# Kernel tuning notes

Hardware: AMD Instinct MI355X
Metric: run time of the kernel (lower is better)

The kernel has to match this reference:

```python
import jax, jax.numpy as jnp
import numpy as np
from jax import lax

HID, STATE, K, EXPAND = 1024, 16, 4, 2
INNER = EXPAND * HID
B_SZ, L = 4, 4096


def setup_inputs() -> dict:
    key = jax.random.key(0)
    ks = jax.random.split(key, 16)
    s = 0.02
    return {
        "x": jax.random.normal(ks[0], (B_SZ, L, HID), dtype=jnp.float32),
        "in_proj_w": jax.random.normal(ks[1], (2 * INNER, HID), dtype=jnp.float32) * s,
        "in_proj_b": jnp.zeros((2 * INNER,), jnp.float32),
        "conv_w": jax.random.normal(ks[2], (INNER, 1, K), dtype=jnp.float32) * s,
        "conv_b": jnp.zeros((INNER,), jnp.float32),
        "dt_w": jax.random.normal(ks[3], (INNER, INNER), dtype=jnp.float32) * s,
        "dt_b": jnp.zeros((INNER,), jnp.float32),
        "A_log": jnp.log(jnp.abs(jax.random.normal(ks[4], (INNER, STATE), dtype=jnp.float32)) + 1e-6),
        "B_w": jax.random.normal(ks[5], (STATE, INNER), dtype=jnp.float32) * s,
        "B_b": jnp.zeros((STATE,), jnp.float32),
        "C_w": jax.random.normal(ks[6], (STATE, INNER), dtype=jnp.float32) * s,
        "C_b": jnp.zeros((STATE,), jnp.float32),
        "D": jnp.ones((INNER,), jnp.float32),
        "out_w": jax.random.normal(ks[7], (HID, INNER), dtype=jnp.float32) * s,
        "out_b": jnp.zeros((HID,), jnp.float32),
    }


def _selective_scan(x, dt, A, Bm, Cm, D):
    # x, dt: (B, L, inner); A: (inner, state); Bm, Cm: (B, L, state); D: (inner,)
    def step(h, inp):
        x_t, dt_t, B_t, C_t = inp  # (B,inner),(B,inner),(B,state),(B,state)
        dA = jnp.exp(dt_t[:, :, None] * A[None, :, :])          # (B, inner, state)
        dB = dt_t[:, :, None] * B_t[:, None, :]                  # (B, inner, state)
        h = dA * h + dB * x_t[:, :, None]
        y = jnp.einsum("bds,bs->bd", h, C_t) + D * x_t
        return h, y

    B_, _, d = x.shape
    h0 = jnp.zeros((B_, d, A.shape[1]), x.dtype)
    xs = (jnp.swapaxes(x, 0, 1), jnp.swapaxes(dt, 0, 1),
          jnp.swapaxes(Bm, 0, 1), jnp.swapaxes(Cm, 0, 1))
    _, ys = lax.scan(step, h0, xs)  # ys: (L, B, inner)
    return jnp.swapaxes(ys, 0, 1)


def reference(x, in_proj_w, in_proj_b, conv_w, conv_b, dt_w, dt_b,
              A_log, B_w, B_b, C_w, C_b, D, out_w, out_b):
    xz = x @ in_proj_w.T + in_proj_b                 # (B, L, 2*inner)
    x_part, z = jnp.split(xz, 2, axis=-1)
    # causal depthwise conv1d: torch pads both sides K-1 then truncates to L -> left pad only
    xc = lax.conv_general_dilated(
        jnp.swapaxes(x_part, 1, 2), conv_w,
        window_strides=(1,), padding=[(K - 1, 0)],
        dimension_numbers=("NCH", "OIH", "NCH"),
        feature_group_count=INNER) + conv_b[None, :, None]
    x_conv = jax.nn.silu(jnp.swapaxes(xc, 1, 2))     # (B, L, inner)
    A = -jnp.exp(A_log)
    dt = jax.nn.softplus(x_conv @ dt_w.T + dt_b)
    Bm = x_conv @ B_w.T + B_b                        # (B, L, state)
    Cm = x_conv @ C_w.T + C_b
    y = _selective_scan(x_conv, dt, A, Bm, Cm, D)
    y = y * jax.nn.silu(z)
    return y @ out_w.T + out_b
```

## Files before the change

kernel.cpp:

```cpp
#include <hip/hip_runtime.h>
#include <hip/hip_bf16.h>

#define HID   1024
#define STATE 16
#define KCONV 4
#define INNER 2048
#define BSZ   4
#define LSEQ  4096
#define BL    (BSZ * LSEQ)
#define NCAT  2176
#define NCH   64
#define TC    64

typedef unsigned short ushort_t;
typedef unsigned int   uint_t;
typedef __attribute__((ext_vector_type(8))) __bf16 bf16x8;
typedef __attribute__((ext_vector_type(4))) float  f32x4;
typedef __attribute__((ext_vector_type(8))) unsigned short u16x8;

__device__ __forceinline__ ushort_t f2bf(float f) {
    uint_t u = __float_as_uint(f);
    u += 0x7fffu + ((u >> 16) & 1u);
    return (ushort_t)(u >> 16);
}
__device__ __forceinline__ float bf2f(ushort_t h) {
    return __uint_as_float(((uint_t)h) << 16);
}

#define AS1 __attribute__((address_space(1)))
#define AS3 __attribute__((address_space(3)))
__device__ __forceinline__ void async_copy16(const ushort_t* g, ushort_t* l) {
    __builtin_amdgcn_global_load_lds((const AS1 void*)g, (AS3 void*)l, 16, 0, 0);
}

__global__ void cast_bf16_kernel(const float* __restrict__ src, ushort_t* __restrict__ dst, int n) {
    int i = blockIdx.x * 256 + threadIdx.x;
    if (i < n) dst[i] = f2bf(src[i]);
}

__global__ void build_wcat_kernel(const float* __restrict__ dtw, const float* __restrict__ Bw,
                                  const float* __restrict__ Cw, ushort_t* __restrict__ out) {
    int i = blockIdx.x * 256 + threadIdx.x;
    if (i >= NCAT * INNER) return;
    int r = i >> 11;
    int k = i & (INNER - 1);
    float v = 0.f;
    if (r < INNER)            v = dtw[i];
    else if (r < INNER + 16)  v = Bw[(r - INNER) * INNER + k];
    else if (r < INNER + 32)  v = Cw[(r - INNER - 16) * INNER + k];
    out[i] = f2bf(v);
}

__global__ void build_biascat_kernel(const float* __restrict__ dtb, const float* __restrict__ Bb,
                                     const float* __restrict__ Cb, float* __restrict__ out) {
    int i = blockIdx.x * 256 + threadIdx.x;
    if (i >= NCAT) return;
    float v = 0.f;
    if (i < INNER)            v = dtb[i];
    else if (i < INNER + 16)  v = Bb[i - INNER];
    else if (i < INNER + 32)  v = Cb[i - INNER - 16];
    out[i] = v;
}

#define mfma_bf16 __builtin_amdgcn_mfma_f32_16x16x32_bf16

template <int MODE, int KK>
__global__ __launch_bounds__(512, 2) void gemm256_kernel(
    const ushort_t* __restrict__ A, const ushort_t* __restrict__ Bw,
    const float* __restrict__ bias,
    ushort_t* __restrict__ oU0, ushort_t* __restrict__ oU1,
    float* __restrict__ oF, float* __restrict__ oB, float* __restrict__ oC,
    int N)
{
    __shared__ ushort_t smem[49152];

    const int tid  = threadIdx.x;
    const int w    = tid >> 6;
    const int lane = tid & 63;
    const int m16  = lane & 15;
    const int ko   = lane >> 4;
    const int wm   = w >> 2;
    const int wn   = w & 3;

    const int gx   = gridDim.x;
    const int lb   = blockIdx.y * gx + blockIdx.x;
    const int xcd  = lb & 7;
    const int slot = lb >> 3;
    const int tx   = slot % gx;
    const int ty   = xcd * 8 + slot / gx;
    const int row0 = ty * 256;
    const int col0 = tx * 128;

    constexpr int NKT = KK >> 6;

    const size_t Lofs = (size_t)(w * 16 + (lane >> 3)) * KK
                      + (size_t)(((lane & 7) ^ (lane >> 3)) << 3);
    const ushort_t* pA = A  + (size_t)row0 * KK + Lofs;
    const ushort_t* pB = Bw + (size_t)col0 * KK + Lofs;

    f32x4 acc[8][2] = {};

    auto stage_tile = [&](int tau) {
        const int bb = (tau & 1) * 24576;
        const int k0 = tau << 6;
#pragma unroll
        for (int j = 0; j < 3; j++) {
            const ushort_t* px = (j == 0) ? pB : pA + (size_t)((j - 1) << 7) * KK;
#pragma unroll
            for (int i = 0; i < 2; i++) {
                const ushort_t* s = px + (size_t)(i * 8) * KK + k0;
                async_copy16(s, &smem[bb + j * 8192 + w * 1024 + i * 512]);
            }
        }
    };
    auto ldA = [&](int buf, int rf, int s) -> bf16x8 {
        const int row = (rf << 4) + m16;
        const int c16 = ((s << 2) + ko) ^ (row & 7);
        return *(const bf16x8*)&smem[buf * 24576 + (1 + wm) * 8192 + (row << 6) + (c16 << 3)];
    };
    auto ldB = [&](int buf, int cf, int s) -> bf16x8 {
        const int row = (wn << 5) + (cf << 4) + m16;
        const int c16 = ((s << 2) + ko) ^ (row & 7);
        return *(const bf16x8*)&smem[buf * 24576 + (row << 6) + (c16 << 3)];
    };

    stage_tile(0);
    asm volatile("s_waitcnt vmcnt(0)" ::: "memory");
    __builtin_amdgcn_s_barrier();

#pragma unroll 1
    for (int t = 0; t < NKT; ++t) {
        const int buf = t & 1;
        if (t + 1 < NKT) stage_tile(t + 1);

#pragma unroll
        for (int s = 0; s < 2; s++) {
            const bf16x8 b0 = ldB(buf, 0, s);
            const bf16x8 b1 = ldB(buf, 1, s);
#pragma unroll
            for (int rf = 0; rf < 8; rf++) {
                const bf16x8 a = ldA(buf, rf, s);
                acc[rf][0] = mfma_bf16(a, b0, acc[rf][0], 0, 0, 0);
                acc[rf][1] = mfma_bf16(a, b1, acc[rf][1], 0, 0, 0);
            }
        }
        if (t + 1 < NKT) {
            asm volatile("s_waitcnt vmcnt(0)" ::: "memory");
            __builtin_amdgcn_s_barrier();
        }
    }

    const int rbase = (lane >> 4) * 4;
    __syncthreads();

    if (MODE == 2) {
#pragma unroll
        for (int rf = 0; rf < 8; rf++)
#pragma unroll
            for (int cf = 0; cf < 2; cf++)
#pragma unroll
                for (int r = 0; r < 4; r++) {
                    int row = row0 + wm * 128 + rf * 16 + rbase + r;
                    int col = col0 + wn * 32 + cf * 16 + m16;
                    oF[(size_t)row * N + col] = acc[rf][cf][r] + bias[col];
                }
    } else if (MODE == 1 && col0 >= INNER) {
#pragma unroll
        for (int rf = 0; rf < 8; rf++)
#pragma unroll
            for (int cf = 0; cf < 2; cf++)
#pragma unroll
                for (int r = 0; r < 4; r++) {
                    int row = row0 + wm * 128 + rf * 16 + rbase + r;
                    int col = col0 + wn * 32 + cf * 16 + m16;
                    float v = acc[rf][cf][r] + bias[col];
                    if (col < INNER + 16)      oB[(size_t)row * STATE + (col - INNER)] = v;
                    else if (col < INNER + 32) oC[(size_t)row * STATE + (col - INNER - 16)] = v;
                }
    } else {
        const bool isZ = (MODE == 0) && (col0 >= INNER);
        ushort_t* my = &smem[w * 4608];
        const int SW = 36;
#pragma unroll
        for (int rf = 0; rf < 8; rf++)
#pragma unroll
            for (int cf = 0; cf < 2; cf++)
#pragma unroll
                for (int r = 0; r < 4; r++) {
                    int lr = rf * 16 + rbase + r;
                    int lc = cf * 16 + m16;
                    float v = acc[rf][cf][r] + bias[col0 + wn * 32 + lc];
                    ushort_t o;
                    if (MODE == 0) {
                        if (isZ) { float s = v / (1.f + __expf(-v)); o = f2bf(s); }
                        else     { o = f2bf(v); }
                    } else {
                        float sp = fmaxf(v, 0.f) + log1pf(__expf(-fabsf(v)));
                        o = f2bf(sp);
                    }
                    my[lr * SW + lc] = o;
                }
        __builtin_amdgcn_sched_barrier(0);
#pragma unroll
        for (int it = 0; it < 8; it++) {
            int lr = it * 16 + (lane >> 2);
            u16x8 vv = *(const u16x8*)&my[lr * SW + (lane & 3) * 8];
            int grow = row0 + wm * 128 + lr;
            int gcol = col0 + wn * 32 + (lane & 3) * 8;
            if (MODE == 0 && isZ)
                *(u16x8*)&oU1[(size_t)grow * INNER + (gcol - INNER)] = vv;
            else
                *(u16x8*)&oU0[(size_t)grow * INNER + gcol] = vv;
        }
    }
}

__global__ void conv_silu_kernel(const ushort_t* __restrict__ xp, const float* __restrict__ cw,
                                 const float* __restrict__ cb,
                                 ushort_t* __restrict__ xcbf) {
    int i = blockIdx.x * 256 + threadIdx.x;
    int base = i * 8;
    int d0 = base & (INNER - 1);
    int bl = base >> 11;
    int l  = bl & (LSEQ - 1);

    f32x4 wv[8];
    float acc[8];
#pragma unroll
    for (int j = 0; j < 8; j++) {
        wv[j]  = *(const f32x4*)&cw[(d0 + j) * KCONV];
        acc[j] = cb[d0 + j];
    }
#pragma unroll
    for (int k = 0; k < KCONV; k++) {
        int ls = l - (KCONV - 1) + k;
        if (ls >= 0) {
            u16x8 v = *(const u16x8*)&xp[base + (ls - l) * INNER];
#pragma unroll
            for (int j = 0; j < 8; j++) acc[j] = fmaf(wv[j][k], bf2f(v[j]), acc[j]);
        }
    }
    u16x8 o;
#pragma unroll
    for (int j = 0; j < 8; j++) {
        float s = acc[j] / (1.f + __expf(-acc[j]));
        o[j] = f2bf(s);
    }
    *(u16x8*)&xcbf[base] = o;
}

__global__ __launch_bounds__(256) void scan_pass1(
    const ushort_t* __restrict__ dt, const ushort_t* __restrict__ xc,
    const float* __restrict__ Bm, const float* __restrict__ A_log,
    ushort_t* __restrict__ Pc, float* __restrict__ Sc)
{
    const int b = blockIdx.z;
    const int c = blockIdx.y;
    const int d = blockIdx.x * 256 + threadIdx.x;

    float A[STATE], h[STATE];
    {
        float al[STATE];
#pragma unroll
        for (int q = 0; q < 4; q++)
            *(f32x4*)(al + q * 4) = *(const f32x4*)(A_log + (size_t)d * STATE + q * 4);
#pragma unroll
        for (int s = 0; s < STATE; s++) { A[s] = -__expf(al[s]); h[s] = 0.f; }
    }
    float sdt = 0.f;
    const size_t base = (size_t)b * LSEQ + (size_t)c * TC;

#pragma unroll 2
    for (int t = 0; t < TC; t++) {
        const size_t r = base + t;
        const float dtv = bf2f(dt[r * INNER + d]);
        const float xv  = bf2f(xc[r * INNER + d]);
        const float dtx = dtv * xv;
        float Bv[STATE];
#pragma unroll
        for (int q = 0; q < 4; q++)
            *(f32x4*)(Bv + q * 4) = *(const f32x4*)(Bm + r * STATE + q * 4);
        sdt += dtv;
#pragma unroll
        for (int s = 0; s < STATE; s++) {
            const float dA = __expf(dtv * A[s]);
            h[s] = fmaf(dA, h[s], dtx * Bv[s]);
        }
    }

    const size_t idx = ((size_t)(b * NCH + c) * INNER + d) * STATE;
#pragma unroll
    for (int q = 0; q < 4; q++)
        *(f32x4*)(Sc + idx + q * 4) = *(const f32x4*)(h + q * 4);
    u16x8 p0, p1;
#pragma unroll
    for (int s = 0; s < 8; s++) { p0[s] = f2bf(__expf(A[s] * sdt)); }
#pragma unroll
    for (int s = 0; s < 8; s++) { p1[s] = f2bf(__expf(A[s + 8] * sdt)); }
    *(u16x8*)(Pc + idx)     = p0;
    *(u16x8*)(Pc + idx + 8) = p1;
}

__global__ __launch_bounds__(256) void scan_pass2(
    const ushort_t* __restrict__ Pc, float* Sc)
{
    const int i = blockIdx.x * 256 + threadIdx.x;
    const int b   = i >> 15;
    const int rem = i & (INNER * STATE - 1);
    float H = 0.f;
#pragma unroll 8
    for (int c = 0; c < NCH; c++) {
        const size_t idx = (size_t)(b * NCH + c) * (INNER * STATE) + rem;
        const float Pv = bf2f(Pc[idx]);
        const float Sv = Sc[idx];
        const float Hn = fmaf(Pv, H, Sv);
        Sc[idx] = H;
        H = Hn;
    }
}

__global__ __launch_bounds__(256) void scan_pass3(
    const ushort_t* __restrict__ dt, const ushort_t* __restrict__ xc,
    const float* __restrict__ Bm, const float* __restrict__ Cm,
    const float* __restrict__ A_log, const float* __restrict__ Dv,
    const float* __restrict__ Hc, ushort_t* sz_y)
{
    const int b = blockIdx.z;
    const int c = blockIdx.y;
    const int d = blockIdx.x * 256 + threadIdx.x;

    float A[STATE], h[STATE];
    {
        float al[STATE];
#pragma unroll
        for (int q = 0; q < 4; q++)
            *(f32x4*)(al + q * 4) = *(const f32x4*)(A_log + (size_t)d * STATE + q * 4);
#pragma unroll
        for (int s = 0; s < STATE; s++) A[s] = -__expf(al[s]);
    }
    const size_t hidx = ((size_t)(b * NCH + c) * INNER + d) * STATE;
#pragma unroll
    for (int q = 0; q < 4; q++)
        *(f32x4*)(h + q * 4) = *(const f32x4*)(Hc + hidx + q * 4);

    const float Dd = Dv[d];
    const size_t base = (size_t)b * LSEQ + (size_t)c * TC;

#pragma unroll 2
    for (int t = 0; t < TC; t++) {
        const size_t r = base + t;
        const float dtv = bf2f(dt[r * INNER + d]);
        const float xv  = bf2f(xc[r * INNER + d]);
        const float dtx = dtv * xv;
        float Bv[STATE], Cv[STATE];
#pragma unroll
        for (int q = 0; q < 4; q++) {
            *(f32x4*)(Bv + q * 4) = *(const f32x4*)(Bm + r * STATE + q * 4);
            *(f32x4*)(Cv + q * 4) = *(const f32x4*)(Cm + r * STATE + q * 4);
        }
        float y = Dd * xv;
#pragma unroll
        for (int s = 0; s < STATE; s++) {
            const float dA = __expf(dtv * A[s]);
            h[s] = fmaf(dA, h[s], dtx * Bv[s]);
            y = fmaf(h[s], Cv[s], y);
        }
        const float zv = bf2f(sz_y[r * INNER + d]);
        sz_y[r * INNER + d] = f2bf(y * zv);
    }
}

extern "C" void kernel_launch(void* const* d_in, const int* in_sizes, int n_in,
                              void* d_out, int out_size, void* d_ws, size_t ws_size,
                              hipStream_t stream) {
    const float* x       = (const float*)d_in[0];
    const float* in_w    = (const float*)d_in[1];
    const float* in_b    = (const float*)d_in[2];
    const float* conv_w  = (const float*)d_in[3];
    const float* conv_b  = (const float*)d_in[4];
    const float* dt_w    = (const float*)d_in[5];
    const float* dt_b    = (const float*)d_in[6];
    const float* A_log   = (const float*)d_in[7];
    const float* B_w     = (const float*)d_in[8];
    const float* B_b     = (const float*)d_in[9];
    const float* C_w     = (const float*)d_in[10];
    const float* C_b     = (const float*)d_in[11];
    const float* Dv      = (const float*)d_in[12];
    const float* out_w   = (const float*)d_in[13];
    const float* out_b   = (const float*)d_in[14];
    float* out = (float*)d_out;

    char* ws = (char*)d_ws;
    size_t off = 0;
    auto alloc = [&](size_t bytes) { size_t o = off; off += (bytes + 255) & ~(size_t)255; return o; };

    ushort_t* Xbf     = (ushort_t*)(ws + alloc((size_t)BL * HID * 2));
    ushort_t* W1bf    = (ushort_t*)(ws + alloc((size_t)2 * INNER * HID * 2));
    ushort_t* Wcat    = (ushort_t*)(ws + alloc((size_t)NCAT * INNER * 2));
    ushort_t* Woutbf  = (ushort_t*)(ws + alloc((size_t)HID * INNER * 2));
    float*    biascat = (float*)   (ws + alloc((size_t)NCAT * 4));
    ushort_t* xpart   = (ushort_t*)(ws + alloc((size_t)BL * INNER * 2));
    ushort_t* szbf    = (ushort_t*)(ws + alloc((size_t)BL * INNER * 2));
    ushort_t* xconvbf = (ushort_t*)(ws + alloc((size_t)BL * INNER * 2));
    float*    Bmbuf   = (float*)   (ws + alloc((size_t)BL * STATE * 4));
    float*    Cmbuf   = (float*)   (ws + alloc((size_t)BL * STATE * 4));
    ushort_t* dtbuf   = xpart;

    ushort_t* Pbuf = (ushort_t*)ws;
    float*    Sbuf = (float*)(ws + (size_t)NCH * BSZ * INNER * STATE * 2);
    (void)in_sizes; (void)n_in; (void)out_size;

    if (ws_size < off) return;

    {
        int n = BL * HID;
        cast_bf16_kernel<<<(n + 255) / 256, 256, 0, stream>>>(x, Xbf, n);
        n = 2 * INNER * HID;
        cast_bf16_kernel<<<(n + 255) / 256, 256, 0, stream>>>(in_w, W1bf, n);
        n = HID * INNER;
        cast_bf16_kernel<<<(n + 255) / 256, 256, 0, stream>>>(out_w, Woutbf, n);
        n = NCAT * INNER;
        build_wcat_kernel<<<(n + 255) / 256, 256, 0, stream>>>(dt_w, B_w, C_w, Wcat);
        build_biascat_kernel<<<(NCAT + 255) / 256, 256, 0, stream>>>(dt_b, B_b, C_b, biascat);
    }

    gemm256_kernel<0, HID><<<dim3((2 * INNER) / 128, BL / 256), 512, 0, stream>>>(
        Xbf, W1bf, in_b, xpart, szbf, nullptr, nullptr, nullptr, 2 * INNER);

    conv_silu_kernel<<<(BL * INNER / 8) / 256, 256, 0, stream>>>(xpart, conv_w, conv_b, xconvbf);

    gemm256_kernel<1, INNER><<<dim3(NCAT / 128, BL / 256), 512, 0, stream>>>(
        xconvbf, Wcat, biascat, dtbuf, nullptr, nullptr, Bmbuf, Cmbuf, NCAT);

    scan_pass1<<<dim3(INNER / 256, NCH, BSZ), 256, 0, stream>>>(
        dtbuf, xconvbf, Bmbuf, A_log, Pbuf, Sbuf);
    scan_pass2<<<(BSZ * INNER * STATE) / 256, 256, 0, stream>>>(Pbuf, Sbuf);
    scan_pass3<<<dim3(INNER / 256, NCH, BSZ), 256, 0, stream>>>(
        dtbuf, xconvbf, Bmbuf, Cmbuf, A_log, Dv, Sbuf, szbf);

    gemm256_kernel<2, INNER><<<dim3(HID / 128, BL / 256), 512, 0, stream>>>(
        szbf, Woutbf, out_b, nullptr, nullptr, out, nullptr, nullptr, HID);
}
```

Before: 1.055 ms.

## Interleave per-slot async loads with MFMA phases using barriers and setprio

Restructures the GEMM main loop into four MFMA phases, each preceded by LDS fragment reads and a per-slot async global-to-LDS copy for the next tiles. The B slot is issued two tiles ahead, and the wait becomes vmcnt(2) so outstanding loads overlap compute. s_setprio raises wave priority during MFMA bursts, in the style of ping-pong scheduling. This adds many extra s_barriers per iteration, and writing buffer slots while other waves may still be reading them is a correctness and synchronisation risk.

```diff
diff --git a/kernel.cpp b/kernel.cpp
--- a/kernel.cpp
+++ b/kernel.cpp
@@ -100,17 +100,14 @@
 
     f32x4 acc[8][2] = {};
 
-    auto stage_tile = [&](int tau) {
+    auto stage_slot = [&](int j, int tau) {
         const int bb = (tau & 1) * 24576;
         const int k0 = tau << 6;
-#pragma unroll
-        for (int j = 0; j < 3; j++) {
-            const ushort_t* px = (j == 0) ? pB : pA + (size_t)((j - 1) << 7) * KK;
-#pragma unroll
-            for (int i = 0; i < 2; i++) {
-                const ushort_t* s = px + (size_t)(i * 8) * KK + k0;
-                async_copy16(s, &smem[bb + j * 8192 + w * 1024 + i * 512]);
-            }
+        const ushort_t* px = (j == 0) ? pB : pA + (size_t)((j - 1) << 7) * KK;
+#pragma unroll
+        for (int i = 0; i < 2; i++) {
+            async_copy16(px + (size_t)(i * 8) * KK + k0,
+                         &smem[bb + j * 8192 + w * 1024 + i * 512]);
         }
     };
     auto ldA = [&](int buf, int rf, int s) -> bf16x8 {
@@ -124,28 +121,65 @@
         return *(const bf16x8*)&smem[buf * 24576 + (row << 6) + (c16 << 3)];
     };
 
-    stage_tile(0);
-    asm volatile("s_waitcnt vmcnt(0)" ::: "memory");
+    stage_slot(0, 0); stage_slot(1, 0); stage_slot(2, 0);
+    stage_slot(0, 1);
+    asm volatile("s_waitcnt vmcnt(2)" ::: "memory");
     __builtin_amdgcn_s_barrier();
 
 #pragma unroll 1
     for (int t = 0; t < NKT; ++t) {
         const int buf = t & 1;
-        if (t + 1 < NKT) stage_tile(t + 1);
-
-#pragma unroll
-        for (int s = 0; s < 2; s++) {
-            const bf16x8 b0 = ldB(buf, 0, s);
-            const bf16x8 b1 = ldB(buf, 1, s);
-#pragma unroll
-            for (int rf = 0; rf < 8; rf++) {
-                const bf16x8 a = ldA(buf, rf, s);
-                acc[rf][0] = mfma_bf16(a, b0, acc[rf][0], 0, 0, 0);
-                acc[rf][1] = mfma_bf16(a, b1, acc[rf][1], 0, 0, 0);
-            }
-        }
+        bf16x8 aF[4][2], b0[2], b1[2];
+
+#pragma unroll
+        for (int rf = 0; rf < 4; rf++) { aF[rf][0] = ldA(buf, rf, 0); aF[rf][1] = ldA(buf, rf, 1); }
+        b0[0] = ldB(buf, 0, 0); b0[1] = ldB(buf, 0, 1);
+        if (t + 1 < NKT) stage_slot(1, t + 1);
+        __builtin_amdgcn_s_barrier();
+        __builtin_amdgcn_s_setprio(1);
+#pragma unroll
+        for (int rf = 0; rf < 4; rf++) {
+            acc[rf][0] = mfma_bf16(aF[rf][0], b0[0], acc[rf][0], 0, 0, 0);
+            acc[rf][0] = mfma_bf16(aF[rf][1], b0[1], acc[rf][0], 0, 0, 0);
+        }
+        __builtin_amdgcn_s_setprio(0);
+        __builtin_amdgcn_s_barrier();
+
+        b1[0] = ldB(buf, 1, 0); b1[1] = ldB(buf, 1, 1);
+        if (t + 1 < NKT) stage_slot(2, t + 1);
+        __builtin_amdgcn_s_barrier();
+        __builtin_amdgcn_s_setprio(1);
+#pragma unroll
+        for (int rf = 0; rf < 4; rf++) {
+            acc[rf][1] = mfma_bf16(aF[rf][0], b1[0], acc[rf][1], 0, 0, 0);
+            acc[rf][1] = mfma_bf16(aF[rf][1], b1[1], acc[rf][1], 0, 0, 0);
+        }
+        __builtin_amdgcn_s_setprio(0);
+        __builtin_amdgcn_s_barrier();
+
+#pragma unroll
+        for (int rf = 0; rf < 4; rf++) { aF[rf][0] = ldA(buf, 4 + rf, 0); aF[rf][1] = ldA(buf, 4 + rf, 1); }
+        if (t + 2 < NKT) stage_slot(0, t + 2);
+        __builtin_amdgcn_s_barrier();
+        __builtin_amdgcn_s_setprio(1);
+#pragma unroll
+        for (int rf = 0; rf < 4; rf++) {
+            acc[4 + rf][1] = mfma_bf16(aF[rf][0], b1[0], acc[4 + rf][1], 0, 0, 0);
+            acc[4 + rf][1] = mfma_bf16(aF[rf][1], b1[1], acc[4 + rf][1], 0, 0, 0);
+        }
+        __builtin_amdgcn_s_setprio(0);
+        __builtin_amdgcn_s_barrier();
+
+        __builtin_amdgcn_s_setprio(1);
+#pragma unroll
+        for (int rf = 0; rf < 4; rf++) {
+            acc[4 + rf][0] = mfma_bf16(aF[rf][0], b0[0], acc[4 + rf][0], 0, 0, 0);
+            acc[4 + rf][0] = mfma_bf16(aF[rf][1], b0[1], acc[4 + rf][0], 0, 0, 0);
+        }
+        __builtin_amdgcn_s_setprio(0);
         if (t + 1 < NKT) {
-            asm volatile("s_waitcnt vmcnt(0)" ::: "memory");
+            if (t + 1 == NKT - 1) asm volatile("s_waitcnt vmcnt(0)" ::: "memory");
+            else                  asm volatile("s_waitcnt vmcnt(2)" ::: "memory");
             __builtin_amdgcn_s_barrier();
         }
     }
```

Result: faster. 1.019 ms (-3.4%).

## Single-buffer GEMM LDS to raise occupancy to four blocks per CU

Applied to the files above, without the earlier changes.

Halves the GEMM shared-memory footprint by dropping the double-buffered K tile in favour of a single buffer with a barrier before and after each stage. Launch bounds change from 2 to 4 blocks per CU. The epilogue LDS transpose is split into two halves so it fits the smaller buffer. The goal is latency hiding through more resident waves instead of software prefetch, but every iteration now waits on global loads with no overlap inside a block, and the tighter register budget may cause spills with the 64-float accumulator.

```diff
diff --git a/kernel.cpp b/kernel.cpp
--- a/kernel.cpp
+++ b/kernel.cpp
@@ -65,14 +65,14 @@
 #define mfma_bf16 __builtin_amdgcn_mfma_f32_16x16x32_bf16
 
 template <int MODE, int KK>
-__global__ __launch_bounds__(512, 2) void gemm256_kernel(
+__global__ __launch_bounds__(512, 4) void gemm256_kernel(
     const ushort_t* __restrict__ A, const ushort_t* __restrict__ Bw,
     const float* __restrict__ bias,
     ushort_t* __restrict__ oU0, ushort_t* __restrict__ oU1,
     float* __restrict__ oF, float* __restrict__ oB, float* __restrict__ oC,
     int N)
 {
-    __shared__ ushort_t smem[49152];
+    __shared__ ushort_t smem[24576];
 
     const int tid  = threadIdx.x;
     const int w    = tid >> 6;
@@ -101,52 +101,45 @@
     f32x4 acc[8][2] = {};
 
     auto stage_tile = [&](int tau) {
-        const int bb = (tau & 1) * 24576;
         const int k0 = tau << 6;
 #pragma unroll
         for (int j = 0; j < 3; j++) {
             const ushort_t* px = (j == 0) ? pB : pA + (size_t)((j - 1) << 7) * KK;
 #pragma unroll
             for (int i = 0; i < 2; i++) {
-                const ushort_t* s = px + (size_t)(i * 8) * KK + k0;
-                async_copy16(s, &smem[bb + j * 8192 + w * 1024 + i * 512]);
+                async_copy16(px + (size_t)(i * 8) * KK + k0,
+                             &smem[j * 8192 + w * 1024 + i * 512]);
             }
         }
     };
-    auto ldA = [&](int buf, int rf, int s) -> bf16x8 {
+    auto ldA = [&](int rf, int s) -> bf16x8 {
         const int row = (rf << 4) + m16;
         const int c16 = ((s << 2) + ko) ^ (row & 7);
-        return *(const bf16x8*)&smem[buf * 24576 + (1 + wm) * 8192 + (row << 6) + (c16 << 3)];
+        return *(const bf16x8*)&smem[(1 + wm) * 8192 + (row << 6) + (c16 << 3)];
     };
-    auto ldB = [&](int buf, int cf, int s) -> bf16x8 {
+    auto ldB = [&](int cf, int s) -> bf16x8 {
         const int row = (wn << 5) + (cf << 4) + m16;
         const int c16 = ((s << 2) + ko) ^ (row & 7);
-        return *(const bf16x8*)&smem[buf * 24576 + (row << 6) + (c16 << 3)];
+        return *(const bf16x8*)&smem[(row << 6) + (c16 << 3)];
     };
-
-    stage_tile(0);
-    asm volatile("s_waitcnt vmcnt(0)" ::: "memory");
-    __builtin_amdgcn_s_barrier();
 
 #pragma unroll 1
     for (int t = 0; t < NKT; ++t) {
-        const int buf = t & 1;
-        if (t + 1 < NKT) stage_tile(t + 1);
+        if (t) __builtin_amdgcn_s_barrier();
+        stage_tile(t);
+        asm volatile("s_waitcnt vmcnt(0)" ::: "memory");
+        __builtin_amdgcn_s_barrier();
 
 #pragma unroll
         for (int s = 0; s < 2; s++) {
-            const bf16x8 b0 = ldB(buf, 0, s);
-            const bf16x8 b1 = ldB(buf, 1, s);
+            const bf16x8 b0 = ldB(0, s);
+            const bf16x8 b1 = ldB(1, s);
 #pragma unroll
             for (int rf = 0; rf < 8; rf++) {
-                const bf16x8 a = ldA(buf, rf, s);
+                const bf16x8 a = ldA(rf, s);
                 acc[rf][0] = mfma_bf16(a, b0, acc[rf][0], 0, 0, 0);
                 acc[rf][1] = mfma_bf16(a, b1, acc[rf][1], 0, 0, 0);
             }
-        }
-        if (t + 1 < NKT) {
-            asm volatile("s_waitcnt vmcnt(0)" ::: "memory");
-            __builtin_amdgcn_s_barrier();
         }
     }
 
@@ -179,38 +172,42 @@
                 }
     } else {
         const bool isZ = (MODE == 0) && (col0 >= INNER);
-        ushort_t* my = &smem[w * 4608];
+        ushort_t* my = &smem[w * 2304];
         const int SW = 36;
 #pragma unroll
-        for (int rf = 0; rf < 8; rf++)
-#pragma unroll
-            for (int cf = 0; cf < 2; cf++)
-#pragma unroll
-                for (int r = 0; r < 4; r++) {
-                    int lr = rf * 16 + rbase + r;
-                    int lc = cf * 16 + m16;
-                    float v = acc[rf][cf][r] + bias[col0 + wn * 32 + lc];
-                    ushort_t o;
-                    if (MODE == 0) {
-                        if (isZ) { float s = v / (1.f + __expf(-v)); o = f2bf(s); }
-                        else     { o = f2bf(v); }
-                    } else {
-                        float sp = fmaxf(v, 0.f) + log1pf(__expf(-fabsf(v)));
-                        o = f2bf(sp);
+        for (int p = 0; p < 2; p++) {
+#pragma unroll
+            for (int rf4 = 0; rf4 < 4; rf4++)
+#pragma unroll
+                for (int cf = 0; cf < 2; cf++)
+#pragma unroll
+                    for (int r = 0; r < 4; r++) {
+                        int lr = rf4 * 16 + rbase + r;
+                        int lc = cf * 16 + m16;
+                        float v = acc[p * 4 + rf4][cf][r] + bias[col0 + wn * 32 + lc];
+                        ushort_t o;
+                        if (MODE == 0) {
+                            if (isZ) { float s = v / (1.f + __expf(-v)); o = f2bf(s); }
+                            else     { o = f2bf(v); }
+                        } else {
+                            float sp = fmaxf(v, 0.f) + log1pf(__expf(-fabsf(v)));
+                            o = f2bf(sp);
+                        }
+                        my[lr * SW + lc] = o;
                     }
-                    my[lr * SW + lc] = o;
-                }
-        __builtin_amdgcn_sched_barrier(0);
-#pragma unroll
-        for (int it = 0; it < 8; it++) {
-            int lr = it * 16 + (lane >> 2);
-            u16x8 vv = *(const u16x8*)&my[lr * SW + (lane & 3) * 8];
-            int grow = row0 + wm * 128 + lr;
-            int gcol = col0 + wn * 32 + (lane & 3) * 8;
-            if (MODE == 0 && isZ)
-                *(u16x8*)&oU1[(size_t)grow * INNER + (gcol - INNER)] = vv;
-            else
-                *(u16x8*)&oU0[(size_t)grow * INNER + gcol] = vv;
+            __builtin_amdgcn_sched_barrier(0);
+#pragma unroll
+            for (int it = 0; it < 4; it++) {
+                int lr = it * 16 + (lane >> 2);
+                u16x8 vv = *(const u16x8*)&my[lr * SW + (lane & 3) * 8];
+                int grow = row0 + wm * 128 + p * 64 + lr;
+                int gcol = col0 + wn * 32 + (lane & 3) * 8;
+                if (MODE == 0 && isZ)
+                    *(u16x8*)&oU1[(size_t)grow * INNER + (gcol - INNER)] = vv;
+                else
+                    *(u16x8*)&oU0[(size_t)grow * INNER + gcol] = vv;
+            }
+            __builtin_amdgcn_sched_barrier(0);
         }
     }
 }
```

After: 925.7 us. -12.3%, faster.
